# Optimization experiments

Measured on AMD Instinct MI355X. Metric: run time of the kernel, lower is better.

The kernel has to match this reference:

```python
import jax, jax.numpy as jnp
import numpy as np

EMBED_DIM = 1024
NUM_HEADS = 16
HEAD_SIZE = EMBED_DIM // NUM_HEADS  # 64
MAX_EMBED_DIM = 2048
MAX_HEAD_SIZE = 128
B, T = 4, 2048


def setup_inputs() -> dict:
    key = jax.random.key(0)
    kx, kq, kk, kv = jax.random.split(key, 4)
    x = jax.random.normal(kx, (B, T, MAX_EMBED_DIM), dtype=jnp.float32)
    # base-head weights sized for the max config; slices are taken in reference()
    Wq = jax.random.normal(kq, (NUM_HEADS, MAX_HEAD_SIZE, MAX_EMBED_DIM), dtype=jnp.float32) * 0.02
    Wk = jax.random.normal(kk, (NUM_HEADS, MAX_HEAD_SIZE, MAX_EMBED_DIM), dtype=jnp.float32) * 0.02
    Wv = jax.random.normal(kv, (NUM_HEADS, MAX_HEAD_SIZE, MAX_EMBED_DIM), dtype=jnp.float32) * 0.02
    return {"x": x, "Wq": Wq, "Wk": Wk, "Wv": Wv}


def reference(x, Wq, Wk, Wv):
    Bx, Tx, _ = x.shape
    xs = x[:, :, :EMBED_DIM]                       # [B, T, E]
    # slice sampled sub-weights: [H, d, E]
    wq = Wq[:, :HEAD_SIZE, :EMBED_DIM]
    wk = Wk[:, :HEAD_SIZE, :EMBED_DIM]
    wv = Wv[:, :HEAD_SIZE, :EMBED_DIM]
    q = jnp.einsum('bte,hde->bhtd', xs, wq)        # [B, H, T, d]
    k = jnp.einsum('bte,hde->bhtd', xs, wk)
    v = jnp.einsum('bte,hde->bhtd', xs, wv)
    scale = jnp.asarray(HEAD_SIZE, x.dtype) ** -0.5
    wei = jnp.einsum('bhtd,bhsd->bhts', q, k) * scale   # [B, H, T, T]
    causal = jnp.tril(jnp.ones((Tx, Tx), dtype=bool))
    wei = jnp.where(causal, wei, jnp.asarray(-jnp.inf, wei.dtype))
    wei = jax.nn.softmax(wei, axis=-1)
    # dropout is identity in eval mode
    out = jnp.einsum('bhts,bhsd->bhtd', wei, v)    # [B, H, T, d]
    out = out.transpose(0, 2, 1, 3).reshape(Bx, Tx, NUM_HEADS * HEAD_SIZE)
    pad = MAX_EMBED_DIM - NUM_HEADS * HEAD_SIZE
    return jnp.pad(out, ((0, 0), (0, 0), (0, pad)))
```

## Files before the change

### kernel.cpp

```cpp
#include <hip/hip_runtime.h>

typedef __attribute__((ext_vector_type(8))) short bf16x8;
typedef __attribute__((ext_vector_type(4))) float f32x4;
typedef __attribute__((ext_vector_type(16))) float f32x16;
typedef __attribute__((ext_vector_type(8))) unsigned short u16x8;
typedef __attribute__((ext_vector_type(4))) unsigned int u32x4;

#define TT 2048

__device__ __forceinline__ unsigned short f2bf(float f) {
  unsigned int u = __builtin_bit_cast(unsigned int, f);
  u += 0x7FFFu + ((u >> 16) & 1u);
  return (unsigned short)(u >> 16);
}

__device__ __forceinline__ void gld16(const void* g, void* l) {
  __builtin_amdgcn_global_load_lds((const __attribute__((address_space(1))) void*)g,
                                   (__attribute__((address_space(3))) void*)l, 16, 0, 0);
}

__device__ __forceinline__ unsigned int cvtpk(float lo, float hi) {
  unsigned int r;
  asm("v_cvt_pk_bf16_f32 %0, %1, %2" : "=v"(r) : "v"(lo), "v"(hi));
  return r;
}

__device__ __forceinline__ void pl32swap(unsigned int& a, unsigned int& b) {
  asm volatile("v_permlane32_swap_b32 %0, %1" : "+v"(a), "+v"(b));
}

__global__ __launch_bounds__(256) void conv_x(const float* __restrict__ x,
                                              unsigned short* __restrict__ xb) {
  const size_t idx = ((size_t)blockIdx.x * 256 + threadIdx.x) * 8;
  const int m = (int)(idx >> 10);
  const int e = (int)(idx & 1023);
  const float4* s = (const float4*)(x + (size_t)m * 2048 + e);
  float4 a = s[0], b = s[1];
  u16x8 v;
  v[0]=f2bf(a.x); v[1]=f2bf(a.y); v[2]=f2bf(a.z); v[3]=f2bf(a.w);
  v[4]=f2bf(b.x); v[5]=f2bf(b.y); v[6]=f2bf(b.z); v[7]=f2bf(b.w);
  *(u16x8*)(xb + idx) = v;
}

__global__ __launch_bounds__(256) void conv_w(const float* __restrict__ Wq,
                                              const float* __restrict__ Wk,
                                              const float* __restrict__ Wv,
                                              unsigned short* __restrict__ wb) {
  const size_t idx = ((size_t)blockIdx.x * 256 + threadIdx.x) * 8;
  const int n = (int)(idx >> 10);
  const int e = (int)(idx & 1023);
  const int mat = n >> 10, hh = (n >> 6) & 15, d = n & 63;
  const float* W = (mat == 0) ? Wq : ((mat == 1) ? Wk : Wv);
  const float4* s = (const float4*)(W + ((size_t)hh * 128 + d) * 2048 + e);
  float4 a = s[0], b = s[1];
  u16x8 v;
  v[0]=f2bf(a.x); v[1]=f2bf(a.y); v[2]=f2bf(a.z); v[3]=f2bf(a.w);
  v[4]=f2bf(b.x); v[5]=f2bf(b.y); v[6]=f2bf(b.z); v[7]=f2bf(b.w);
  *(u16x8*)(wb + idx) = v;
}

__global__ __launch_bounds__(256) void qkv_gemm(const unsigned short* __restrict__ xb,
                                                const unsigned short* __restrict__ wb,
                                                unsigned short* __restrict__ Q,
                                                unsigned short* __restrict__ Kt,
                                                unsigned short* __restrict__ Vt) {
  __shared__ unsigned short As[128 * 64];
  __shared__ unsigned short Bs[128 * 64];
  const int tid = threadIdx.x;
  const int w = tid >> 6, lane = tid & 63, g = lane >> 4, c = lane & 15;
  const int m0 = blockIdx.x * 128;
  const int n0 = blockIdx.y * 128;

  f32x4 acc[2][8];
#pragma unroll
  for (int mi = 0; mi < 2; ++mi)
#pragma unroll
    for (int ni = 0; ni < 8; ++ni) acc[mi][ni] = (f32x4){0.f, 0.f, 0.f, 0.f};

  for (int kt = 0; kt < 16; ++kt) {
    const int k0 = kt * 64;
#pragma unroll
    for (int it = 0; it < 4; ++it) {
      int o = (it * 256 + tid) * 16;
      int r = o >> 7, c2 = o & 127;
      int c2s = c2 ^ ((r & 7) << 4);
      gld16(xb + ((size_t)(m0 + r) * 1024 + k0 + (c2s >> 1)), (char*)As + o);
      gld16(wb + ((size_t)(n0 + r) * 1024 + k0 + (c2s >> 1)), (char*)Bs + o);
    }
    __syncthreads();
#pragma unroll
    for (int kk = 0; kk < 2; ++kk) {
      bf16x8 af[2], bfr[8];
#pragma unroll
      for (int mi = 0; mi < 2; ++mi) {
        int r = w * 32 + mi * 16 + c;
        int c2s = (kk * 64 + g * 16) ^ ((r & 7) << 4);
        af[mi] = *(const bf16x8*)&As[r * 64 + (c2s >> 1)];
      }
#pragma unroll
      for (int ni = 0; ni < 8; ++ni) {
        int r = ni * 16 + c;
        int c2s = (kk * 64 + g * 16) ^ ((r & 7) << 4);
        bfr[ni] = *(const bf16x8*)&Bs[r * 64 + (c2s >> 1)];
      }
#pragma unroll
      for (int mi = 0; mi < 2; ++mi)
#pragma unroll
        for (int ni = 0; ni < 8; ++ni)
          acc[mi][ni] = __builtin_amdgcn_mfma_f32_16x16x32_bf16(af[mi], bfr[ni], acc[mi][ni], 0, 0, 0);
    }
    __syncthreads();
  }

#pragma unroll
  for (int mi = 0; mi < 2; ++mi) {
    const int row_l = w * 32 + mi * 16 + g * 4;
#pragma unroll
    for (int i = 0; i < 4; ++i) {
      const int m = m0 + row_l + i;
      const int b = m >> 11, t = m & 2047;
#pragma unroll
      for (int ni = 0; ni < 8; ++ni) {
        const int n = n0 + ni * 16 + c;
        const int mat = n >> 10, hh = (n >> 6) & 15, d = n & 63;
        const unsigned short v = f2bf(acc[mi][ni][i]);
        const size_t bh = (size_t)(b * 16 + hh);
        if (mat == 0)      Q [(bh * TT + t) * 64 + d] = v;
        else if (mat == 1) Kt[(bh * TT + t) * 64 + d] = v;
        else               Vt[(bh * 64 + d) * TT + t] = v;
      }
    }
  }
}

__global__ __launch_bounds__(256) void zero_pad(float* __restrict__ out) {
  const int idx = blockIdx.x * 256 + threadIdx.x;
  const int row = idx >> 8, c4 = idx & 255;
  *((float4*)(out + (size_t)row * 2048 + 1024) + c4) = make_float4(0.f, 0.f, 0.f, 0.f);
}

__global__ __launch_bounds__(256) void attn4(const unsigned short* __restrict__ Q,
                                             const unsigned short* __restrict__ K,
                                             const unsigned short* __restrict__ Vt,
                                             float* __restrict__ out) {
  __shared__ unsigned short Ks[2][4096];
  __shared__ unsigned short Vs[2][4096];
  const int blk = blockIdx.x;
  const int bh = blk & 63;
  const int qi = 15 - (blk >> 6);
  const int b = bh >> 4, h = bh & 15;
  const int tid = threadIdx.x;
  const int w = tid >> 6, lane = tid & 63;
  const int ql = lane & 31;
  const int hi = lane >> 5, hi8 = hi * 8;
  const int q0 = qi * 128;
  const int qw = q0 + w * 32;
  const int q = qw + ql;
  const unsigned short* Qp = Q  + (size_t)bh * TT * 64;
  const unsigned short* Kp = K  + (size_t)bh * TT * 64;
  const unsigned short* Vp = Vt + (size_t)bh * 64 * TT;

  bf16x8 qf0, qf1, qf2, qf3;
  {
    const unsigned short* qa = Qp + (size_t)q * 64 + hi8;
    qf0 = *(const bf16x8*)(qa);
    qf1 = *(const bf16x8*)(qa + 16);
    qf2 = *(const bf16x8*)(qa + 32);
    qf3 = *(const bf16x8*)(qa + 48);
  }

  f32x16 o0, o1;
#pragma unroll
  for (int r = 0; r < 16; ++r) { o0[r] = 0.f; o1[r] = 0.f; }
  float m = -3.0e38f, l = 0.f;
  const float c2 = 0.125f * 1.44269504f;

  const int nt = qi * 2 + 2;

  auto STAGE = [&](int t, int buf) {
#pragma unroll
    for (int it = 0; it < 2; ++it) {
      const int o = (it * 256 + tid) * 16;
      const int r = o >> 7, c = o & 127;
      const int cs = c ^ ((r & 7) << 4);
      gld16(Kp + (size_t)t * 4096 + r * 64 + (cs >> 1), (char*)&Ks[buf][0] + o);
      gld16(Vp + (size_t)r * 2048 + t * 64 + (cs >> 1), (char*)&Vs[buf][0] + o);
    }
  };

  STAGE(0, 0);
  asm volatile("s_waitcnt vmcnt(0)" ::: "memory");
  __syncthreads();

  int cur = 0;
  for (int t = 0; t < nt; ++t) {
    if (t + 1 < nt) STAGE(t + 1, cur ^ 1);

#pragma unroll
    for (int s = 0; s < 2; ++s) {
      const int ks32 = t * 64 + s * 32;
      if (ks32 <= qw) {
        const int krow = s * 32 + ql;
        const char* kb = (const char*)&Ks[cur][krow * 64];
        const int ksz = (krow & 7) << 4;
        bf16x8 kf0 = *(const bf16x8*)(kb + ((0  + hi * 16) ^ ksz));
        bf16x8 kf1 = *(const bf16x8*)(kb + ((32 + hi * 16) ^ ksz));
        bf16x8 kf2 = *(const bf16x8*)(kb + ((64 + hi * 16) ^ ksz));
        bf16x8 kf3 = *(const bf16x8*)(kb + ((96 + hi * 16) ^ ksz));
        const int vsz = (ql & 7) << 4;
        const char* vb0 = (const char*)&Vs[cur][ql * 64];
        const char* vb1 = (const char*)&Vs[cur][(ql + 32) * 64];
        bf16x8 vf0 = *(const bf16x8*)(vb0 + ((s * 64 + 0  + hi * 16) ^ vsz));
        bf16x8 vf1 = *(const bf16x8*)(vb0 + ((s * 64 + 32 + hi * 16) ^ vsz));
        bf16x8 vf2 = *(const bf16x8*)(vb1 + ((s * 64 + 0  + hi * 16) ^ vsz));
        bf16x8 vf3 = *(const bf16x8*)(vb1 + ((s * 64 + 32 + hi * 16) ^ vsz));

        f32x16 st;
#pragma unroll
        for (int r = 0; r < 16; ++r) st[r] = 0.f;
        __builtin_amdgcn_s_setprio(1);
        st = __builtin_amdgcn_mfma_f32_32x32x16_bf16(kf0, qf0, st, 0, 0, 0);
        st = __builtin_amdgcn_mfma_f32_32x32x16_bf16(kf1, qf1, st, 0, 0, 0);
        st = __builtin_amdgcn_mfma_f32_32x32x16_bf16(kf2, qf2, st, 0, 0, 0);
        st = __builtin_amdgcn_mfma_f32_32x32x16_bf16(kf3, qf3, st, 0, 0, 0);
        __builtin_amdgcn_s_setprio(0);

        if (ks32 == qw) {
#pragma unroll
          for (int r = 0; r < 16; ++r) {
            const int krw = (r & 3) + 8 * (r >> 2) + 4 * hi;
            if (krw > ql) st[r] = -3.0e38f;
          }
        }

        float t0 = fmaxf(st[0], st[1]),  t1 = fmaxf(st[2], st[3]);
        float t2 = fmaxf(st[4], st[5]),  t3 = fmaxf(st[6], st[7]);
        float t4 = fmaxf(st[8], st[9]),  t5 = fmaxf(st[10], st[11]);
        float t6 = fmaxf(st[12], st[13]), t7 = fmaxf(st[14], st[15]);
        t0 = fmaxf(t0, t1); t2 = fmaxf(t2, t3); t4 = fmaxf(t4, t5); t6 = fmaxf(t6, t7);
        float pm = fmaxf(fmaxf(t0, t2), fmaxf(t4, t6));
        pm = fmaxf(pm, __shfl_xor(pm, 32));
        if (!__all(pm - m <= 44.36f)) {
          const float mnew = fmaxf(m, pm);
          const float alpha = __builtin_amdgcn_exp2f((m - mnew) * c2);
          m = mnew;
          l *= alpha;
#pragma unroll
          for (int r = 0; r < 16; ++r) { o0[r] *= alpha; o1[r] *= alpha; }
        }
        float p[16];
        float rs = 0.f;
#pragma unroll
        for (int r = 0; r < 16; ++r) {
          p[r] = __builtin_amdgcn_exp2f((st[r] - m) * c2);
          rs += p[r];
        }
        rs += __shfl_xor(rs, 32);
        l += rs;

        unsigned int a0 = cvtpk(p[0], p[1]),  a1 = cvtpk(p[2], p[3]);
        unsigned int b0 = cvtpk(p[4], p[5]),  b1 = cvtpk(p[6], p[7]);
        pl32swap(a0, b0); pl32swap(a1, b1);
        unsigned int cc0 = cvtpk(p[8], p[9]),  cc1 = cvtpk(p[10], p[11]);
        unsigned int dd0 = cvtpk(p[12], p[13]), dd1 = cvtpk(p[14], p[15]);
        pl32swap(cc0, dd0); pl32swap(cc1, dd1);
        u32x4 pw0 = {a0, a1, b0, b1};
        u32x4 pw1 = {cc0, cc1, dd0, dd1};
        bf16x8 pf0 = __builtin_bit_cast(bf16x8, pw0);
        bf16x8 pf1 = __builtin_bit_cast(bf16x8, pw1);

        __builtin_amdgcn_s_setprio(1);
        o0 = __builtin_amdgcn_mfma_f32_32x32x16_bf16(vf0, pf0, o0, 0, 0, 0);
        o0 = __builtin_amdgcn_mfma_f32_32x32x16_bf16(vf1, pf1, o0, 0, 0, 0);
        o1 = __builtin_amdgcn_mfma_f32_32x32x16_bf16(vf2, pf0, o1, 0, 0, 0);
        o1 = __builtin_amdgcn_mfma_f32_32x32x16_bf16(vf3, pf1, o1, 0, 0, 0);
        __builtin_amdgcn_s_setprio(0);
      }
    }

    asm volatile("s_waitcnt vmcnt(0)" ::: "memory");
    __syncthreads();
    cur ^= 1;
  }

  const float inv = 1.f / l;
  float* ob = out + ((size_t)b * TT + q) * 2048 + h * 64;
#pragma unroll
  for (int r = 0; r < 16; ++r) {
    const int row = (r & 3) + 8 * (r >> 2) + 4 * hi;
    ob[row]      = o0[r] * inv;
    ob[32 + row] = o1[r] * inv;
  }
}

extern "C" void kernel_launch(void* const* d_in, const int* in_sizes, int n_in,
                              void* d_out, int out_size, void* d_ws, size_t ws_size,
                              hipStream_t stream) {
  const float* x  = (const float*)d_in[0];
  const float* Wq = (const float*)d_in[1];
  const float* Wk = (const float*)d_in[2];
  const float* Wv = (const float*)d_in[3];

  unsigned short* wsp = (unsigned short*)d_ws;
  unsigned short* Q   = wsp;
  unsigned short* Kt  = wsp + (size_t)8388608;
  unsigned short* Vt  = wsp + (size_t)16777216;

  unsigned short* xb = (unsigned short*)d_out;
  unsigned short* wb = (unsigned short*)((char*)d_out + 33554432);
  float* out = (float*)d_out;

  conv_x<<<4096, 256, 0, stream>>>(x, xb);
  conv_w<<<1536, 256, 0, stream>>>(Wq, Wk, Wv, wb);
  qkv_gemm<<<dim3(64, 24), 256, 0, stream>>>(xb, wb, Q, Kt, Vt);
  zero_pad<<<8192, 256, 0, stream>>>(out);
  attn4<<<1024, 256, 0, stream>>>(Q, Kt, Vt, out);
}
```

Before: 183.2 us.

## Double-buffer QKV GEMM with larger tiles and fold zero padding into attention

Rewrites the QKV projection GEMM to use 512-thread blocks with a 128x256 tile and a two-stage LDS prefetch pipeline, so global loads for the next k-tiles overlap MFMA work. It also raises wave priority around the MFMA bursts. The separate zero_pad kernel is removed and each attention block writes zeros into its own slice of the padded output columns, saving a launch. Larger LDS usage may lower occupancy.

Measured after the change: 157.7 us. -13.9%, faster.

```diff
diff --git a/kernel.cpp b/kernel.cpp
--- a/kernel.cpp
+++ b/kernel.cpp
@@ -59,84 +59,103 @@
   *(u16x8*)(wb + idx) = v;
 }
 
-__global__ __launch_bounds__(256) void qkv_gemm(const unsigned short* __restrict__ xb,
-                                                const unsigned short* __restrict__ wb,
-                                                unsigned short* __restrict__ Q,
-                                                unsigned short* __restrict__ Kt,
-                                                unsigned short* __restrict__ Vt) {
-  __shared__ unsigned short As[128 * 64];
-  __shared__ unsigned short Bs[128 * 64];
+__global__ __launch_bounds__(512) void qkv_gemm2(const unsigned short* __restrict__ xb,
+                                                 const unsigned short* __restrict__ wb,
+                                                 unsigned short* __restrict__ Q,
+                                                 unsigned short* __restrict__ Kt,
+                                                 unsigned short* __restrict__ Vt) {
+  __shared__ unsigned short As[2][128 * 64];
+  __shared__ unsigned short Bs[2][256 * 64];
   const int tid = threadIdx.x;
   const int w = tid >> 6, lane = tid & 63, g = lane >> 4, c = lane & 15;
+  const int wm = w >> 2, wn = w & 3;
   const int m0 = blockIdx.x * 128;
-  const int n0 = blockIdx.y * 128;
-
-  f32x4 acc[2][8];
-#pragma unroll
-  for (int mi = 0; mi < 2; ++mi)
-#pragma unroll
-    for (int ni = 0; ni < 8; ++ni) acc[mi][ni] = (f32x4){0.f, 0.f, 0.f, 0.f};
-
-  for (int kt = 0; kt < 16; ++kt) {
-    const int k0 = kt * 64;
+  const int n0 = blockIdx.y * 256;
+
+  f32x4 acc[4][4];
+#pragma unroll
+  for (int mi = 0; mi < 4; ++mi)
+#pragma unroll
+    for (int ni = 0; ni < 4; ++ni) acc[mi][ni] = (f32x4){0.f, 0.f, 0.f, 0.f};
+
+  auto STAGE = [&](int t, int buf) {
+    const int k0 = t * 64;
+#pragma unroll
+    for (int it = 0; it < 2; ++it) {
+      const int o = (it * 512 + tid) * 16;
+      const int r = o >> 7, cc = o & 127;
+      const int cs = cc ^ ((r & 7) << 4);
+      gld16(xb + ((size_t)(m0 + r) << 10) + k0 + (cs >> 1), (char*)&As[buf][0] + o);
+    }
 #pragma unroll
     for (int it = 0; it < 4; ++it) {
-      int o = (it * 256 + tid) * 16;
-      int r = o >> 7, c2 = o & 127;
-      int c2s = c2 ^ ((r & 7) << 4);
-      gld16(xb + ((size_t)(m0 + r) * 1024 + k0 + (c2s >> 1)), (char*)As + o);
-      gld16(wb + ((size_t)(n0 + r) * 1024 + k0 + (c2s >> 1)), (char*)Bs + o);
-    }
-    __syncthreads();
+      const int o = (it * 512 + tid) * 16;
+      const int r = o >> 7, cc = o & 127;
+      const int cs = cc ^ ((r & 7) << 4);
+      gld16(wb + ((size_t)(n0 + r) << 10) + k0 + (cs >> 1), (char*)&Bs[buf][0] + o);
+    }
+  };
+
+  STAGE(0, 0);
+  STAGE(1, 1);
+  asm volatile("s_waitcnt vmcnt(6)" ::: "memory");
+  __builtin_amdgcn_s_barrier();
+
+  for (int t = 0; t < 16; ++t) {
+    const int cur = t & 1;
 #pragma unroll
     for (int kk = 0; kk < 2; ++kk) {
-      bf16x8 af[2], bfr[8];
-#pragma unroll
-      for (int mi = 0; mi < 2; ++mi) {
-        int r = w * 32 + mi * 16 + c;
-        int c2s = (kk * 64 + g * 16) ^ ((r & 7) << 4);
-        af[mi] = *(const bf16x8*)&As[r * 64 + (c2s >> 1)];
+      bf16x8 af[4], bfv[4];
+#pragma unroll
+      for (int mi = 0; mi < 4; ++mi) {
+        const int r = wm * 64 + mi * 16 + c;
+        const int cs = (kk * 64 + g * 16) ^ ((r & 7) << 4);
+        af[mi] = *(const bf16x8*)((const char*)&As[cur][r * 64] + cs);
       }
 #pragma unroll
-      for (int ni = 0; ni < 8; ++ni) {
-        int r = ni * 16 + c;
-        int c2s = (kk * 64 + g * 16) ^ ((r & 7) << 4);
-        bfr[ni] = *(const bf16x8*)&Bs[r * 64 + (c2s >> 1)];
+      for (int ni = 0; ni < 4; ++ni) {
+        const int r = wn * 64 + ni * 16 + c;
+        const int cs = (kk * 64 + g * 16) ^ ((r & 7) << 4);
+        bfv[ni] = *(const bf16x8*)((const char*)&Bs[cur][r * 64] + cs);
       }
-#pragma unroll
-      for (int mi = 0; mi < 2; ++mi)
-#pragma unroll
-        for (int ni = 0; ni < 8; ++ni)
-          acc[mi][ni] = __builtin_amdgcn_mfma_f32_16x16x32_bf16(af[mi], bfr[ni], acc[mi][ni], 0, 0, 0);
-    }
-    __syncthreads();
-  }
-
-#pragma unroll
-  for (int mi = 0; mi < 2; ++mi) {
-    const int row_l = w * 32 + mi * 16 + g * 4;
+      __builtin_amdgcn_s_setprio(1);
+#pragma unroll
+      for (int mi = 0; mi < 4; ++mi)
+#pragma unroll
+        for (int ni = 0; ni < 4; ++ni)
+          acc[mi][ni] = __builtin_amdgcn_mfma_f32_16x16x32_bf16(af[mi], bfv[ni], acc[mi][ni], 0, 0, 0);
+      __builtin_amdgcn_s_setprio(0);
+    }
+    __builtin_amdgcn_s_barrier();
+    if (t + 2 < 16) {
+      STAGE(t + 2, cur);
+      asm volatile("s_waitcnt vmcnt(6)" ::: "memory");
+      __builtin_amdgcn_s_barrier();
+    } else if (t + 1 < 16) {
+      asm volatile("s_waitcnt vmcnt(0)" ::: "memory");
+      __builtin_amdgcn_s_barrier();
+    }
+  }
+
+#pragma unroll
+  for (int mi = 0; mi < 4; ++mi) {
+    const int row_l = wm * 64 + mi * 16 + g * 4;
 #pragma unroll
     for (int i = 0; i < 4; ++i) {
       const int m = m0 + row_l + i;
-      const int b = m >> 11, t = m & 2047;
-#pragma unroll
-      for (int ni = 0; ni < 8; ++ni) {
-        const int n = n0 + ni * 16 + c;
+      const int b = m >> 11, tt = m & 2047;
+#pragma unroll
+      for (int ni = 0; ni < 4; ++ni) {
+        const int n = n0 + wn * 64 + ni * 16 + c;
         const int mat = n >> 10, hh = (n >> 6) & 15, d = n & 63;
         const unsigned short v = f2bf(acc[mi][ni][i]);
         const size_t bh = (size_t)(b * 16 + hh);
-        if (mat == 0)      Q [(bh * TT + t) * 64 + d] = v;
-        else if (mat == 1) Kt[(bh * TT + t) * 64 + d] = v;
-        else               Vt[(bh * 64 + d) * TT + t] = v;
+        if (mat == 0)      Q [(bh * TT + tt) * 64 + d] = v;
+        else if (mat == 1) Kt[(bh * TT + tt) * 64 + d] = v;
+        else               Vt[(bh * 64 + d) * TT + tt] = v;
       }
     }
   }
-}
-
-__global__ __launch_bounds__(256) void zero_pad(float* __restrict__ out) {
-  const int idx = blockIdx.x * 256 + threadIdx.x;
-  const int row = idx >> 8, c4 = idx & 255;
-  *((float4*)(out + (size_t)row * 2048 + 1024) + c4) = make_float4(0.f, 0.f, 0.f, 0.f);
 }
 
 __global__ __launch_bounds__(256) void attn4(const unsigned short* __restrict__ Q,
@@ -291,6 +310,14 @@
     ob[row]      = o0[r] * inv;
     ob[32 + row] = o1[r] * inv;
   }
+
+  const float4 z = make_float4(0.f, 0.f, 0.f, 0.f);
+#pragma unroll
+  for (int it = 0; it < 8; ++it) {
+    const int idx = it * 256 + tid;
+    const int r = idx >> 4, c4 = idx & 15;
+    *((float4*)(out + ((size_t)b * TT + q0 + r) * 2048 + 1024 + h * 64) + c4) = z;
+  }
 }
 
 extern "C" void kernel_launch(void* const* d_in, const int* in_sizes, int n_in,
@@ -312,7 +339,6 @@
 
   conv_x<<<4096, 256, 0, stream>>>(x, xb);
   conv_w<<<1536, 256, 0, stream>>>(Wq, Wk, Wv, wb);
-  qkv_gemm<<<dim3(64, 24), 256, 0, stream>>>(xb, wb, Q, Kt, Vt);
-  zero_pad<<<8192, 256, 0, stream>>>(out);
+  qkv_gemm2<<<dim3(64, 12), 512, 0, stream>>>(xb, wb, Q, Kt, Vt);
   attn4<<<1024, 256, 0, stream>>>(Q, Kt, Vt, out);
 }
```
